# Performance work log

Measured on AMD Instinct MI355X. Metric: run time of the kernel, lower is better.

## Reference

```python
import jax, jax.numpy as jnp
import numpy as np

NUM_CLASSES = 80
IOU_THR = 0.5
CLS_GAIN, OBJ_GAIN, BBOX_GAIN = 0.5, 1.0, 0.05


def _bce_logits(logits, targets):
    # stable BCEWithLogits, elementwise (reduction='none')
    return jnp.maximum(logits, 0.0) - logits * targets + jnp.log1p(jnp.exp(-jnp.abs(logits)))


def _cxcywh_to_xyxy(b):
    cx, cy, w, h = b[..., 0], b[..., 1], b[..., 2], b[..., 3]
    return jnp.stack([cx - w / 2, cy - h / 2, cx + w / 2, cy + h / 2], axis=-1)


def _ciou_loss(pred_cxcywh, tgt_cxcywh):
    p = _cxcywh_to_xyxy(pred_cxcywh)
    t = _cxcywh_to_xyxy(tgt_cxcywh)
    ix1 = jnp.maximum(p[:, 0], t[:, 0]); iy1 = jnp.maximum(p[:, 1], t[:, 1])
    ix2 = jnp.minimum(p[:, 2], t[:, 2]); iy2 = jnp.minimum(p[:, 3], t[:, 3])
    inter = jnp.clip(ix2 - ix1, 0.0) * jnp.clip(iy2 - iy1, 0.0)
    a1 = (p[:, 2] - p[:, 0]) * (p[:, 3] - p[:, 1])
    a2 = (t[:, 2] - t[:, 0]) * (t[:, 3] - t[:, 1])
    iou = inter / (a1 + a2 - inter + 1e-7)
    pcx = (p[:, 0] + p[:, 2]) / 2; pcy = (p[:, 1] + p[:, 3]) / 2
    tcx = (t[:, 0] + t[:, 2]) / 2; tcy = (t[:, 1] + t[:, 3]) / 2
    cd = (pcx - tcx) ** 2 + (pcy - tcy) ** 2
    ex1 = jnp.minimum(p[:, 0], t[:, 0]); ey1 = jnp.minimum(p[:, 1], t[:, 1])
    ex2 = jnp.maximum(p[:, 2], t[:, 2]); ey2 = jnp.maximum(p[:, 3], t[:, 3])
    dd = (ex2 - ex1) ** 2 + (ey2 - ey1) ** 2
    return 1.0 - (iou - cd / (dd + 1e-7))


def _layer_losses(pred, boxes, labels, valid, anchors_l):
    # pred: [B, A, gh, gw, 5+nc]; boxes: [B, M, 4] xyxy normalized
    B, A, gh, gw, C = pred.shape
    nc = C - 5
    x1, y1, x2, y2 = boxes[..., 0], boxes[..., 1], boxes[..., 2], boxes[..., 3]
    cx = (x1 + x2) * 0.5 * gw
    cy = (y1 + y2) * 0.5 * gh
    w = (x2 - x1) * gw
    h = (y2 - y1) * gh
    # wh-only IoU against this layer's anchors -> best anchor per box
    inter = jnp.minimum(w[..., None], anchors_l[:, 0]) * jnp.minimum(h[..., None], anchors_l[:, 1])
    union = (w * h)[..., None] + anchors_l[:, 0] * anchors_l[:, 1] - inter
    ious = inter / (union + 1e-6)                       # [B, M, A]
    best_iou = ious.max(axis=-1)
    best_a = jnp.argmax(ious, axis=-1)
    pos = valid & (best_iou > IOU_THR)                  # [B, M]
    gx = jnp.clip(cx.astype(jnp.int32), 0, gw - 1)
    gy = jnp.clip(cy.astype(jnp.int32), 0, gh - 1)
    b_idx = jnp.broadcast_to(jnp.arange(B)[:, None], pos.shape)
    flat = lambda a: a.reshape(-1)
    b_f, a_f, gy_f, gx_f = flat(b_idx), flat(best_a), flat(gy), flat(gx)
    m = flat(pos).astype(pred.dtype)                    # [B*M]
    npos = m.sum()
    denom = jnp.maximum(npos, 1.0)
    pred_pos = pred[b_f, a_f, gy_f, gx_f]               # [B*M, C]
    onehot = jax.nn.one_hot(flat(labels), nc, dtype=pred.dtype)
    cls = (_bce_logits(pred_pos[:, 5:], onehot) * m[:, None]).sum() / (denom * nc)
    tbox = jnp.stack([flat(cx), flat(cy), flat(w), flat(h)], axis=-1)
    bbox = (_ciou_loss(pred_pos[:, :4], tbox) * m).sum() / denom
    obj_t = jnp.zeros((B, A, gh, gw), pred.dtype).at[b_f, a_f, gy_f, gx_f].max(m)
    obj = _bce_logits(pred[..., 4], obj_t).mean()
    has = (npos > 0).astype(pred.dtype)                 # layer skipped entirely if no positives
    return has * cls, has * obj, has * bbox


def reference(p3, p4, p5, boxes, labels, valid, anchors):
    cls_l = obj_l = box_l = jnp.asarray(0.0, p3.dtype)
    for i, pred in enumerate((p3, p4, p5)):
        c, o, b = _layer_losses(pred, boxes, labels, valid, anchors[i])
        cls_l = cls_l + c
        obj_l = obj_l + o
        box_l = box_l + b
    return CLS_GAIN * cls_l + OBJ_GAIN * obj_l + BBOX_GAIN * box_l


def setup_inputs() -> dict:
    key = jax.random.key(0)
    ks = jax.random.split(key, 8)
    B, M = 16, 64
    p3 = jax.random.normal(ks[0], (B, 3, 80, 80, 85), jnp.float32)
    p4 = jax.random.normal(ks[1], (B, 3, 40, 40, 85), jnp.float32)
    p5 = jax.random.normal(ks[2], (B, 3, 20, 20, 85), jnp.float32)
    cx = jax.random.uniform(ks[3], (B, M), minval=0.2, maxval=0.8)
    cy = jax.random.uniform(ks[4], (B, M), minval=0.2, maxval=0.8)
    wh = jax.random.uniform(ks[5], (B, M, 2), minval=0.05, maxval=0.4)
    boxes = jnp.stack([cx - wh[..., 0] / 2, cy - wh[..., 1] / 2,
                       cx + wh[..., 0] / 2, cy + wh[..., 1] / 2], axis=-1).astype(jnp.float32)
    labels = jax.random.randint(ks[6], (B, M), 0, NUM_CLASSES, jnp.int32)
    valid = jax.random.bernoulli(ks[7], 0.8, (B, M))
    anchors = jnp.array([[[10, 13], [16, 30], [33, 23]],
                         [[30, 61], [62, 45], [59, 119]],
                         [[116, 90], [156, 198], [373, 326]]], jnp.float32)
    return {"p3": p3, "p4": p4, "p5": p5, "boxes": boxes,
            "labels": labels, "valid": valid, "anchors": anchors}
```

## Files before the change

kernel.cpp:

```cpp
#include <hip/hip_runtime.h>
#include <hip/hip_bf16.h>


#define NCLS 80
#define NCH 85
#define REC_IDX_OFF 256
#define REC_META_OFF 3328
#define OBJ_BLOCKS 394
#define CLS_BLOCKS 240
#define TOT_BLOCKS (OBJ_BLOCKS + CLS_BLOCKS)

__device__ __forceinline__ float bce0(float x) {
    return fmaxf(x, 0.0f) + log1pf(expf(-fabsf(x)));
}

__device__ __forceinline__ float ciou_loss(float px, float py, float pw, float ph,
                                           float tx, float ty, float tw, float th) {
    float p0 = px - pw * 0.5f, p1 = py - ph * 0.5f, p2 = px + pw * 0.5f, p3 = py + ph * 0.5f;
    float t0 = tx - tw * 0.5f, t1 = ty - th * 0.5f, t2 = tx + tw * 0.5f, t3 = ty + th * 0.5f;
    float ix1 = fmaxf(p0, t0), iy1 = fmaxf(p1, t1);
    float ix2 = fminf(p2, t2), iy2 = fminf(p3, t3);
    float inter = fmaxf(ix2 - ix1, 0.0f) * fmaxf(iy2 - iy1, 0.0f);
    float a1 = (p2 - p0) * (p3 - p1);
    float a2 = (t2 - t0) * (t3 - t1);
    float iou = inter / (a1 + a2 - inter + 1e-7f);
    float pcx = (p0 + p2) * 0.5f, pcy = (p1 + p3) * 0.5f;
    float tcx = (t0 + t2) * 0.5f, tcy = (t1 + t3) * 0.5f;
    float cd = (pcx - tcx) * (pcx - tcx) + (pcy - tcy) * (pcy - tcy);
    float ex1 = fminf(p0, t0), ey1 = fminf(p1, t1);
    float ex2 = fmaxf(p2, t2), ey2 = fmaxf(p3, t3);
    float dd = (ex2 - ex1) * (ex2 - ex1) + (ey2 - ey1) * (ey2 - ey1);
    return 1.0f - (iou - cd / (dd + 1e-7f));
}

__global__ __launch_bounds__(1024) void k1(
    const float* __restrict__ p3, const float* __restrict__ p4, const float* __restrict__ p5,
    const float* __restrict__ boxes, const int* __restrict__ labels,
    const unsigned char* __restrict__ validb, const float* __restrict__ anchors,
    float* __restrict__ ws)
{
    __shared__ int s_info[3][1024];
    __shared__ float s_acc[12];
    __shared__ int s_nrec;
    __shared__ int s_nz[4];
    __shared__ int s_flag;

    int* ws_i = (int*)ws;
    const int t = threadIdx.x;
    if (t < 12) s_acc[t] = 0.0f;
    if (t == 0) s_nrec = 0;
    if (t < 4) s_nz[t] = 0;
    __syncthreads();

    if (t < 256) {
        int nz = 0;
#pragma unroll
        for (int j = 0; j < 4; j++) if (validb[t * 4 + j]) nz |= (1 << j);
        if (nz & 1) atomicOr(&s_nz[0], 1);
        if (nz & 2) atomicOr(&s_nz[1], 1);
        if (nz & 4) atomicOr(&s_nz[2], 1);
        if (nz & 8) atomicOr(&s_nz[3], 1);
    }
    __syncthreads();
    if (t == 0) {
        int f;
        if (!s_nz[1] && !s_nz[2] && !s_nz[3]) f = 0;
        else if (!s_nz[0] && !s_nz[1]) f = 2;
        else f = 1;
        s_flag = f;
    }
    __syncthreads();
    const int flag = s_flag;

    const int b = t >> 6;
    const int m = t & 63;
    const float x1 = boxes[t * 4 + 0], y1 = boxes[t * 4 + 1];
    const float x2 = boxes[t * 4 + 2], y2 = boxes[t * 4 + 3];
    bool valid;
    if (flag == 0)      valid = ((const int*)validb)[t] != 0;
    else if (flag == 1) valid = validb[t] != 0;
    else                valid = ((const float*)validb)[t] != 0.0f;
    const int label = labels[t];

    const int GDIM[3] = {80, 40, 20};
    float cxl[3], cyl[3], wl[3], hl[3];
    int infol[3];
#pragma unroll
    for (int l = 0; l < 3; l++) {
        const float g = (float)GDIM[l];
        const float cx = (x1 + x2) * 0.5f * g;
        const float cy = (y1 + y2) * 0.5f * g;
        const float w = (x2 - x1) * g;
        const float h = (y2 - y1) * g;
        float best = -1.0f; int ba = 0;
#pragma unroll
        for (int a = 0; a < 3; a++) {
            const float aw = anchors[l * 6 + a * 2 + 0];
            const float ah = anchors[l * 6 + a * 2 + 1];
            const float inter = fminf(w, aw) * fminf(h, ah);
            const float uni = w * h + aw * ah - inter;
            const float iou = inter / (uni + 1e-6f);
            if (iou > best) { best = iou; ba = a; }
        }
        const bool pos = valid && (best > 0.5f);
        int gx = (int)cx; gx = gx < 0 ? 0 : (gx > GDIM[l] - 1 ? GDIM[l] - 1 : gx);
        int gy = (int)cy; gy = gy < 0 ? 0 : (gy > GDIM[l] - 1 ? GDIM[l] - 1 : gy);
        const int info = (pos ? (1 << 16) : 0) | (ba << 14) | (gy << 7) | gx;
        s_info[l][t] = info;
        infol[l] = info; cxl[l] = cx; cyl[l] = cy; wl[l] = w; hl[l] = h;
    }
    __syncthreads();

#pragma unroll
    for (int l = 0; l < 3; l++) {
        const int info = infol[l];
        if (info & (1 << 16)) {
            const int ba = (info >> 14) & 3, gy = (info >> 7) & 127, gx = info & 127;
            const int g = GDIM[l];
            const int idx = (((b * 3 + ba) * g + gy) * g + gx) * NCH;
            const float* base = (l == 0) ? p3 : ((l == 1) ? p4 : p5);
            atomicAdd(&s_acc[l], 1.0f);
            const float bb = ciou_loss(base[idx + 0], base[idx + 1], base[idx + 2], base[idx + 3],
                                       cxl[l], cyl[l], wl[l], hl[l]);
            atomicAdd(&s_acc[6 + l], bb);
            bool dup = false;
            const int rowbase = b * 64;
            for (int mm = 0; mm < m; mm++) {
                if (s_info[l][rowbase + mm] == info) { dup = true; break; }
            }
            if (!dup) atomicAdd(&s_acc[9 + l], base[idx + 4]);
            const int r = atomicAdd(&s_nrec, 1);
            ws_i[REC_IDX_OFF + r] = idx;
            ws_i[REC_META_OFF + r] = label | (l << 16);
        }
    }
    __syncthreads();

    if (t < 12) ws[t] = s_acc[t];
    if (t >= 12 && t < 15) ws[t] = 0.0f;
    if (t == 15) ws_i[15] = s_nrec;
}

__global__ __launch_bounds__(256) void k2(
    const float* __restrict__ p3, const float* __restrict__ p4, const float* __restrict__ p5,
    float* __restrict__ ws)
{
    int* ws_i = (int*)ws;
    const int blk = blockIdx.x, t = threadIdx.x;

    if (blk < OBJ_BLOCKS) {
        int layer, cell0, ncell;
        const float* base;
        if (blk < 300)      { layer = 0; cell0 = blk * 1024;         ncell = 307200; base = p3; }
        else if (blk < 375) { layer = 1; cell0 = (blk - 300) * 1024; ncell = 76800;  base = p4; }
        else                { layer = 2; cell0 = (blk - 375) * 1024; ncell = 19200;  base = p5; }
        float acc = 0.0f;
#pragma unroll
        for (int k = 0; k < 4; k++) {
            const int cell = cell0 + k * 256 + t;
            if (cell < ncell) acc += bce0(base[(size_t)cell * NCH + 4]);
        }
#pragma unroll
        for (int off = 32; off > 0; off >>= 1) acc += __shfl_down(acc, off);
        __shared__ float s[4];
        if ((t & 63) == 0) s[t >> 6] = acc;
        __syncthreads();
        if (t == 0) atomicAdd(&ws[12 + layer], s[0] + s[1] + s[2] + s[3]);
    } else {
        const int P = ws_i[15];
        const int total = P * NCLS;
        float a0 = 0.0f, a1 = 0.0f, a2 = 0.0f;
#pragma unroll
        for (int k = 0; k < 4; k++) {
            const int job = (blk - OBJ_BLOCKS) * 1024 + k * 256 + t;
            if (job < total) {
                const int r = job / NCLS;
                const int c = job - r * NCLS;
                const int idx = ws_i[REC_IDX_OFF + r];
                const int meta = ws_i[REC_META_OFF + r];
                const int l = meta >> 16;
                const int lab = meta & 0xFFFF;
                const float* base = (l == 0) ? p3 : ((l == 1) ? p4 : p5);
                const float logit = base[idx + 5 + c];
                const float tv = (c == lab) ? 1.0f : 0.0f;
                const float bce = fmaxf(logit, 0.0f) - logit * tv + log1pf(expf(-fabsf(logit)));
                a0 += (l == 0) ? bce : 0.0f;
                a1 += (l == 1) ? bce : 0.0f;
                a2 += (l == 2) ? bce : 0.0f;
            }
        }
#pragma unroll
        for (int off = 32; off > 0; off >>= 1) {
            a0 += __shfl_down(a0, off);
            a1 += __shfl_down(a1, off);
            a2 += __shfl_down(a2, off);
        }
        __shared__ float s3[4][3];
        if ((t & 63) == 0) { s3[t >> 6][0] = a0; s3[t >> 6][1] = a1; s3[t >> 6][2] = a2; }
        __syncthreads();
        if (t == 0) {
            const float c0 = s3[0][0] + s3[1][0] + s3[2][0] + s3[3][0];
            const float c1 = s3[0][1] + s3[1][1] + s3[2][1] + s3[3][1];
            const float c2 = s3[0][2] + s3[1][2] + s3[2][2] + s3[3][2];
            if (c0 != 0.0f) atomicAdd(&ws[3], c0);
            if (c1 != 0.0f) atomicAdd(&ws[4], c1);
            if (c2 != 0.0f) atomicAdd(&ws[5], c2);
        }
    }
}

__global__ void k3(const float* __restrict__ ws, float* __restrict__ out) {
    float cls = 0.0f, obj = 0.0f, box = 0.0f;
    const float GRID[3] = {307200.0f, 76800.0f, 19200.0f};
    for (int l = 0; l < 3; l++) {
        const float npos = ws[l];
        const float has = npos > 0.0f ? 1.0f : 0.0f;
        const float denom = fmaxf(npos, 1.0f);
        cls += has * ws[3 + l] / (denom * 80.0f);
        box += has * ws[6 + l] / denom;
        obj += has * (ws[12 + l] - ws[9 + l]) / GRID[l];
    }
    out[0] = 0.5f * cls + 1.0f * obj + 0.05f * box;
}

extern "C" void kernel_launch(void* const* d_in, const int* in_sizes, int n_in,
                              void* d_out, int out_size, void* d_ws, size_t ws_size,
                              hipStream_t stream) {
    const float* p3 = (const float*)d_in[0];
    const float* p4 = (const float*)d_in[1];
    const float* p5 = (const float*)d_in[2];
    const float* boxes = (const float*)d_in[3];
    const int* labels = (const int*)d_in[4];
    const unsigned char* validb = (const unsigned char*)d_in[5];
    const float* anchors = (const float*)d_in[6];
    float* ws = (float*)d_ws;
    float* out = (float*)d_out;

    k1<<<1, 1024, 0, stream>>>(p3, p4, p5, boxes, labels, validb, anchors, ws);
    k2<<<TOT_BLOCKS, 256, 0, stream>>>(p3, p4, p5, ws);
    k3<<<1, 1, 0, stream>>>(ws, out);
}
```

Before: 187.7 us.

## Merge target-matching kernel into main loss kernel with per-block partials

Removes the serial single-block matching kernel by recomputing anchor matching inside each class-BCE block and in a few dedicated box-loss blocks, so everything runs in one wide launch. Per-block partial sums are written to workspace instead of atomics, and a 256-thread finalize kernel reduces them. Objectness blocks are halved in size to double the block count. The cost is redundant per-thread matching work and a dense class-job space covering all box/layer slots, not just the positive ones.

```diff
diff --git a/kernel.cpp b/kernel.cpp
--- a/kernel.cpp
+++ b/kernel.cpp
@@ -4,11 +4,12 @@
 
 #define NCLS 80
 #define NCH 85
-#define REC_IDX_OFF 256
-#define REC_META_OFF 3328
-#define OBJ_BLOCKS 394
+#define OBJ_BLOCKS 788
 #define CLS_BLOCKS 240
-#define TOT_BLOCKS (OBJ_BLOCKS + CLS_BLOCKS)
+#define BOX_BLOCKS 4
+#define TOT_BLOCKS (OBJ_BLOCKS + CLS_BLOCKS + BOX_BLOCKS)
+#define OBJ_PART_OFF 64
+#define CLS_PART_OFF 1024
 
 __device__ __forceinline__ float bce0(float x) {
     return fmaxf(x, 0.0f) + log1pf(expf(-fabsf(x)));
@@ -33,130 +34,83 @@
     return 1.0f - (iou - cd / (dd + 1e-7f));
 }
 
-__global__ __launch_bounds__(1024) void k1(
+__device__ __forceinline__ int detect_valid_flag(const unsigned char* validb, int t,
+                                                 int* s_nz, int* s_flag) {
+    if (t < 4) s_nz[t] = 0;
+    __syncthreads();
+    {
+        int nz = 0;
+#pragma unroll
+        for (int j = 0; j < 4; j++) if (validb[t * 4 + j]) nz |= (1 << j);
+        if (nz & 1) atomicOr(&s_nz[0], 1);
+        if (nz & 2) atomicOr(&s_nz[1], 1);
+        if (nz & 4) atomicOr(&s_nz[2], 1);
+        if (nz & 8) atomicOr(&s_nz[3], 1);
+    }
+    __syncthreads();
+    if (t == 0) {
+        int f;
+        if (!s_nz[1] && !s_nz[2] && !s_nz[3]) f = 0;
+        else if (!s_nz[0] && !s_nz[1]) f = 2;
+        else f = 1;
+        *s_flag = f;
+    }
+    __syncthreads();
+    return *s_flag;
+}
+
+__device__ __forceinline__ bool read_valid(const unsigned char* validb, int bm, int flag) {
+    if (flag == 0) return ((const int*)validb)[bm] != 0;
+    if (flag == 1) return validb[bm] != 0;
+    return ((const float*)validb)[bm] != 0.0f;
+}
+
+__device__ __forceinline__ void match_box(
+    const float* __restrict__ boxes, const float* __restrict__ anchors,
+    bool valid, int bm, int l, int gdim,
+    bool& pos, int& ba, int& gx, int& gy,
+    float& cx, float& cy, float& w, float& h)
+{
+    const float x1 = boxes[bm * 4 + 0], y1 = boxes[bm * 4 + 1];
+    const float x2 = boxes[bm * 4 + 2], y2 = boxes[bm * 4 + 3];
+    const float g = (float)gdim;
+    cx = (x1 + x2) * 0.5f * g;
+    cy = (y1 + y2) * 0.5f * g;
+    w = (x2 - x1) * g;
+    h = (y2 - y1) * g;
+    float best = -1.0f; ba = 0;
+#pragma unroll
+    for (int a = 0; a < 3; a++) {
+        const float aw = anchors[l * 6 + a * 2 + 0];
+        const float ah = anchors[l * 6 + a * 2 + 1];
+        const float inter = fminf(w, aw) * fminf(h, ah);
+        const float uni = w * h + aw * ah - inter;
+        const float iou = inter / (uni + 1e-6f);
+        if (iou > best) { best = iou; ba = a; }
+    }
+    pos = valid && (best > 0.5f);
+    gx = (int)cx; gx = gx < 0 ? 0 : (gx > gdim - 1 ? gdim - 1 : gx);
+    gy = (int)cy; gy = gy < 0 ? 0 : (gy > gdim - 1 ? gdim - 1 : gy);
+}
+
+__global__ __launch_bounds__(256) void K(
     const float* __restrict__ p3, const float* __restrict__ p4, const float* __restrict__ p5,
     const float* __restrict__ boxes, const int* __restrict__ labels,
     const unsigned char* __restrict__ validb, const float* __restrict__ anchors,
     float* __restrict__ ws)
 {
-    __shared__ int s_info[3][1024];
-    __shared__ float s_acc[12];
-    __shared__ int s_nrec;
-    __shared__ int s_nz[4];
-    __shared__ int s_flag;
-
-    int* ws_i = (int*)ws;
-    const int t = threadIdx.x;
-    if (t < 12) s_acc[t] = 0.0f;
-    if (t == 0) s_nrec = 0;
-    if (t < 4) s_nz[t] = 0;
-    __syncthreads();
-
-    if (t < 256) {
-        int nz = 0;
-#pragma unroll
-        for (int j = 0; j < 4; j++) if (validb[t * 4 + j]) nz |= (1 << j);
-        if (nz & 1) atomicOr(&s_nz[0], 1);
-        if (nz & 2) atomicOr(&s_nz[1], 1);
-        if (nz & 4) atomicOr(&s_nz[2], 1);
-        if (nz & 8) atomicOr(&s_nz[3], 1);
-    }
-    __syncthreads();
-    if (t == 0) {
-        int f;
-        if (!s_nz[1] && !s_nz[2] && !s_nz[3]) f = 0;
-        else if (!s_nz[0] && !s_nz[1]) f = 2;
-        else f = 1;
-        s_flag = f;
-    }
-    __syncthreads();
-    const int flag = s_flag;
-
-    const int b = t >> 6;
-    const int m = t & 63;
-    const float x1 = boxes[t * 4 + 0], y1 = boxes[t * 4 + 1];
-    const float x2 = boxes[t * 4 + 2], y2 = boxes[t * 4 + 3];
-    bool valid;
-    if (flag == 0)      valid = ((const int*)validb)[t] != 0;
-    else if (flag == 1) valid = validb[t] != 0;
-    else                valid = ((const float*)validb)[t] != 0.0f;
-    const int label = labels[t];
-
+    const int blk = blockIdx.x, t = threadIdx.x;
     const int GDIM[3] = {80, 40, 20};
-    float cxl[3], cyl[3], wl[3], hl[3];
-    int infol[3];
-#pragma unroll
-    for (int l = 0; l < 3; l++) {
-        const float g = (float)GDIM[l];
-        const float cx = (x1 + x2) * 0.5f * g;
-        const float cy = (y1 + y2) * 0.5f * g;
-        const float w = (x2 - x1) * g;
-        const float h = (y2 - y1) * g;
-        float best = -1.0f; int ba = 0;
-#pragma unroll
-        for (int a = 0; a < 3; a++) {
-            const float aw = anchors[l * 6 + a * 2 + 0];
-            const float ah = anchors[l * 6 + a * 2 + 1];
-            const float inter = fminf(w, aw) * fminf(h, ah);
-            const float uni = w * h + aw * ah - inter;
-            const float iou = inter / (uni + 1e-6f);
-            if (iou > best) { best = iou; ba = a; }
-        }
-        const bool pos = valid && (best > 0.5f);
-        int gx = (int)cx; gx = gx < 0 ? 0 : (gx > GDIM[l] - 1 ? GDIM[l] - 1 : gx);
-        int gy = (int)cy; gy = gy < 0 ? 0 : (gy > GDIM[l] - 1 ? GDIM[l] - 1 : gy);
-        const int info = (pos ? (1 << 16) : 0) | (ba << 14) | (gy << 7) | gx;
-        s_info[l][t] = info;
-        infol[l] = info; cxl[l] = cx; cyl[l] = cy; wl[l] = w; hl[l] = h;
-    }
-    __syncthreads();
-
-#pragma unroll
-    for (int l = 0; l < 3; l++) {
-        const int info = infol[l];
-        if (info & (1 << 16)) {
-            const int ba = (info >> 14) & 3, gy = (info >> 7) & 127, gx = info & 127;
-            const int g = GDIM[l];
-            const int idx = (((b * 3 + ba) * g + gy) * g + gx) * NCH;
-            const float* base = (l == 0) ? p3 : ((l == 1) ? p4 : p5);
-            atomicAdd(&s_acc[l], 1.0f);
-            const float bb = ciou_loss(base[idx + 0], base[idx + 1], base[idx + 2], base[idx + 3],
-                                       cxl[l], cyl[l], wl[l], hl[l]);
-            atomicAdd(&s_acc[6 + l], bb);
-            bool dup = false;
-            const int rowbase = b * 64;
-            for (int mm = 0; mm < m; mm++) {
-                if (s_info[l][rowbase + mm] == info) { dup = true; break; }
-            }
-            if (!dup) atomicAdd(&s_acc[9 + l], base[idx + 4]);
-            const int r = atomicAdd(&s_nrec, 1);
-            ws_i[REC_IDX_OFF + r] = idx;
-            ws_i[REC_META_OFF + r] = label | (l << 16);
-        }
-    }
-    __syncthreads();
-
-    if (t < 12) ws[t] = s_acc[t];
-    if (t >= 12 && t < 15) ws[t] = 0.0f;
-    if (t == 15) ws_i[15] = s_nrec;
-}
-
-__global__ __launch_bounds__(256) void k2(
-    const float* __restrict__ p3, const float* __restrict__ p4, const float* __restrict__ p5,
-    float* __restrict__ ws)
-{
-    int* ws_i = (int*)ws;
-    const int blk = blockIdx.x, t = threadIdx.x;
 
     if (blk < OBJ_BLOCKS) {
         int layer, cell0, ncell;
         const float* base;
-        if (blk < 300)      { layer = 0; cell0 = blk * 1024;         ncell = 307200; base = p3; }
-        else if (blk < 375) { layer = 1; cell0 = (blk - 300) * 1024; ncell = 76800;  base = p4; }
-        else                { layer = 2; cell0 = (blk - 375) * 1024; ncell = 19200;  base = p5; }
+        if (blk < 600)      { layer = 0; cell0 = blk * 512;         ncell = 307200; base = p3; }
+        else if (blk < 750) { layer = 1; cell0 = (blk - 600) * 512; ncell = 76800;  base = p4; }
+        else                { layer = 2; cell0 = (blk - 750) * 512; ncell = 19200;  base = p5; }
         float acc = 0.0f;
 #pragma unroll
-        for (int k = 0; k < 4; k++) {
+        for (int k = 0; k < 2; k++) {
             const int cell = cell0 + k * 256 + t;
             if (cell < ncell) acc += bce0(base[(size_t)cell * NCH + 4]);
         }
@@ -165,24 +119,29 @@
         __shared__ float s[4];
         if ((t & 63) == 0) s[t >> 6] = acc;
         __syncthreads();
-        if (t == 0) atomicAdd(&ws[12 + layer], s[0] + s[1] + s[2] + s[3]);
-    } else {
-        const int P = ws_i[15];
-        const int total = P * NCLS;
+        if (t == 0) ws[OBJ_PART_OFF + blk] = s[0] + s[1] + s[2] + s[3];
+    } else if (blk < OBJ_BLOCKS + CLS_BLOCKS) {
+        __shared__ int s_nz[4], s_flag;
+        const int flag = detect_valid_flag(validb, t, s_nz, &s_flag);
+        const int cblk = blk - OBJ_BLOCKS;
         float a0 = 0.0f, a1 = 0.0f, a2 = 0.0f;
 #pragma unroll
         for (int k = 0; k < 4; k++) {
-            const int job = (blk - OBJ_BLOCKS) * 1024 + k * 256 + t;
-            if (job < total) {
-                const int r = job / NCLS;
-                const int c = job - r * NCLS;
-                const int idx = ws_i[REC_IDX_OFF + r];
-                const int meta = ws_i[REC_META_OFF + r];
-                const int l = meta >> 16;
-                const int lab = meta & 0xFFFF;
+            const int job = cblk * 1024 + k * 256 + t;
+            const int rec = job / NCLS;
+            const int c = job - rec * NCLS;
+            const int bm = rec / 3;
+            const int l = rec - bm * 3;
+            const bool valid = read_valid(validb, bm, flag);
+            bool pos; int ba, gx, gy; float cx, cy, w, h;
+            match_box(boxes, anchors, valid, bm, l, GDIM[l], pos, ba, gx, gy, cx, cy, w, h);
+            if (pos) {
+                const int b = bm >> 6;
+                const int g = GDIM[l];
+                const int idx = (((b * 3 + ba) * g + gy) * g + gx) * NCH;
                 const float* base = (l == 0) ? p3 : ((l == 1) ? p4 : p5);
                 const float logit = base[idx + 5 + c];
-                const float tv = (c == lab) ? 1.0f : 0.0f;
+                const float tv = (c == labels[bm]) ? 1.0f : 0.0f;
                 const float bce = fmaxf(logit, 0.0f) - logit * tv + log1pf(expf(-fabsf(logit)));
                 a0 += (l == 0) ? bce : 0.0f;
                 a1 += (l == 1) ? bce : 0.0f;
@@ -199,28 +158,90 @@
         if ((t & 63) == 0) { s3[t >> 6][0] = a0; s3[t >> 6][1] = a1; s3[t >> 6][2] = a2; }
         __syncthreads();
         if (t == 0) {
-            const float c0 = s3[0][0] + s3[1][0] + s3[2][0] + s3[3][0];
-            const float c1 = s3[0][1] + s3[1][1] + s3[2][1] + s3[3][1];
-            const float c2 = s3[0][2] + s3[1][2] + s3[2][2] + s3[3][2];
-            if (c0 != 0.0f) atomicAdd(&ws[3], c0);
-            if (c1 != 0.0f) atomicAdd(&ws[4], c1);
-            if (c2 != 0.0f) atomicAdd(&ws[5], c2);
-        }
-    }
-}
-
-__global__ void k3(const float* __restrict__ ws, float* __restrict__ out) {
-    float cls = 0.0f, obj = 0.0f, box = 0.0f;
-    const float GRID[3] = {307200.0f, 76800.0f, 19200.0f};
-    for (int l = 0; l < 3; l++) {
-        const float npos = ws[l];
-        const float has = npos > 0.0f ? 1.0f : 0.0f;
-        const float denom = fmaxf(npos, 1.0f);
-        cls += has * ws[3 + l] / (denom * 80.0f);
-        box += has * ws[6 + l] / denom;
-        obj += has * (ws[12 + l] - ws[9 + l]) / GRID[l];
-    }
-    out[0] = 0.5f * cls + 1.0f * obj + 0.05f * box;
+            ws[CLS_PART_OFF + cblk * 3 + 0] = s3[0][0] + s3[1][0] + s3[2][0] + s3[3][0];
+            ws[CLS_PART_OFF + cblk * 3 + 1] = s3[0][1] + s3[1][1] + s3[2][1] + s3[3][1];
+            ws[CLS_PART_OFF + cblk * 3 + 2] = s3[0][2] + s3[1][2] + s3[2][2] + s3[3][2];
+        }
+    } else {
+        __shared__ int s_nz[4], s_flag;
+        __shared__ int s_info[3][1024];
+        __shared__ float s_bacc[9];
+        const int flag = detect_valid_flag(validb, t, s_nz, &s_flag);
+        if (t < 9) s_bacc[t] = 0.0f;
+#pragma unroll
+        for (int j = 0; j < 4; j++) {
+            const int bm = t + j * 256;
+            const bool valid = read_valid(validb, bm, flag);
+#pragma unroll
+            for (int l = 0; l < 3; l++) {
+                bool pos; int ba, gx, gy; float cx, cy, w, h;
+                match_box(boxes, anchors, valid, bm, l, GDIM[l], pos, ba, gx, gy, cx, cy, w, h);
+                s_info[l][bm] = (pos ? (1 << 16) : 0) | (ba << 14) | (gy << 7) | gx;
+            }
+        }
+        __syncthreads();
+        const int bblk = blk - OBJ_BLOCKS - CLS_BLOCKS;
+        const int bm = bblk * 256 + t;
+        const int b = bm >> 6;
+        const int m = bm & 63;
+        const bool valid = read_valid(validb, bm, flag);
+#pragma unroll
+        for (int l = 0; l < 3; l++) {
+            const int info = s_info[l][bm];
+            if (info & (1 << 16)) {
+                const int ba = (info >> 14) & 3, gy = (info >> 7) & 127, gx = info & 127;
+                const int g = GDIM[l];
+                const int idx = (((b * 3 + ba) * g + gy) * g + gx) * NCH;
+                const float* base = (l == 0) ? p3 : ((l == 1) ? p4 : p5);
+                bool pos; int ba2, gx2, gy2; float cx, cy, w, h;
+                match_box(boxes, anchors, valid, bm, l, GDIM[l], pos, ba2, gx2, gy2, cx, cy, w, h);
+                atomicAdd(&s_bacc[0 + l], 1.0f);
+                const float bb = ciou_loss(base[idx + 0], base[idx + 1], base[idx + 2], base[idx + 3],
+                                           cx, cy, w, h);
+                atomicAdd(&s_bacc[3 + l], bb);
+                bool dup = false;
+                const int rowbase = b * 64;
+                for (int mm = rowbase; mm < rowbase + m; mm++) {
+                    if (s_info[l][mm] == info) { dup = true; break; }
+                }
+                if (!dup) atomicAdd(&s_bacc[6 + l], base[idx + 4]);
+            }
+        }
+        __syncthreads();
+        if (t < 9) ws[bblk * 16 + t] = s_bacc[t];
+    }
+}
+
+__global__ __launch_bounds__(256) void k3(const float* __restrict__ ws, float* __restrict__ out) {
+    __shared__ float s_acc[16];
+    const int t = threadIdx.x;
+    if (t < 16) s_acc[t] = 0.0f;
+    __syncthreads();
+    for (int i = t; i < OBJ_BLOCKS; i += 256) {
+        const int l = (i < 600) ? 0 : ((i < 750) ? 1 : 2);
+        atomicAdd(&s_acc[9 + l], ws[OBJ_PART_OFF + i]);
+    }
+    for (int i = t; i < CLS_BLOCKS * 3; i += 256) {
+        atomicAdd(&s_acc[12 + i % 3], ws[CLS_PART_OFF + i]);
+    }
+    if (t < BOX_BLOCKS * 9) {
+        const int bblk = t / 9, r = t % 9;
+        atomicAdd(&s_acc[r], ws[bblk * 16 + r]);
+    }
+    __syncthreads();
+    if (t == 0) {
+        float cls = 0.0f, obj = 0.0f, box = 0.0f;
+        const float GRID[3] = {307200.0f, 76800.0f, 19200.0f};
+        for (int l = 0; l < 3; l++) {
+            const float npos = s_acc[l];
+            const float has = npos > 0.0f ? 1.0f : 0.0f;
+            const float denom = fmaxf(npos, 1.0f);
+            cls += has * s_acc[12 + l] / (denom * 80.0f);
+            box += has * s_acc[3 + l] / denom;
+            obj += has * (s_acc[9 + l] - s_acc[6 + l]) / GRID[l];
+        }
+        out[0] = 0.5f * cls + 1.0f * obj + 0.05f * box;
+    }
 }
 
 extern "C" void kernel_launch(void* const* d_in, const int* in_sizes, int n_in,
@@ -236,7 +257,6 @@
     float* ws = (float*)d_ws;
     float* out = (float*)d_out;
 
-    k1<<<1, 1024, 0, stream>>>(p3, p4, p5, boxes, labels, validb, anchors, ws);
-    k2<<<TOT_BLOCKS, 256, 0, stream>>>(p3, p4, p5, ws);
-    k3<<<1, 1, 0, stream>>>(ws, out);
-}
+    K<<<TOT_BLOCKS, 256, 0, stream>>>(p3, p4, p5, boxes, labels, validb, anchors, ws);
+    k3<<<1, 256, 0, stream>>>(ws, out);
+}
```

Result: faster. 183.7 us (-2.1%).
